# Optimization experiments

Measured on AMD Instinct MI355X. Metric: run time of the kernel, lower is better.

The kernel has to match this reference:

```python
import jax, jax.numpy as jnp
import numpy as np

N_NODES = 100000
N_EDGES = 1600000
F = 64          # node_features (in == out for EvolveGCNO)
HID = 64        # hidden_size


def setup_inputs() -> dict:
    key = jax.random.key(0)
    ks = jax.random.split(key, 12)
    s = 1.0 / np.sqrt(F)
    inp = {
        "x": jax.random.normal(ks[0], (N_NODES, F), dtype=jnp.float32),
        "edge_index": jax.random.randint(ks[1], (2, N_EDGES), 0, N_NODES, dtype=jnp.int64),
        "edge_weight": jax.random.uniform(ks[2], (N_EDGES,), dtype=jnp.float32),
        # evolving GCN weight (initial_weight of EvolveGCNO)
        "W0": jax.random.uniform(ks[3], (F, F), jnp.float32, -s, s),
        # GRU (input_size=F, hidden_size=F): gates ordered r, z, n
        "gru_Wi": jax.random.uniform(ks[4], (3 * F, F), jnp.float32, -s, s),
        "gru_Wh": jax.random.uniform(ks[5], (3 * F, F), jnp.float32, -s, s),
        "gru_bi": jax.random.uniform(ks[6], (3 * F,), jnp.float32, -s, s),
        "gru_bh": jax.random.uniform(ks[7], (3 * F,), jnp.float32, -s, s),
        # projection F -> HID and head HID -> 1
        "proj_W": jax.random.uniform(ks[8], (HID, F), jnp.float32, -s, s),
        "proj_b": jax.random.uniform(ks[9], (HID,), jnp.float32, -s, s),
        "lin_W": jax.random.uniform(ks[10], (1, HID), jnp.float32, -1.0 / np.sqrt(HID), 1.0 / np.sqrt(HID)),
        "lin_b": jax.random.uniform(ks[11], (1,), jnp.float32, -1.0 / np.sqrt(HID), 1.0 / np.sqrt(HID)),
    }
    return inp


def reference(x, edge_index, edge_weight, W0, gru_Wi, gru_Wh, gru_bi, gru_bh,
              proj_W, proj_b, lin_W, lin_b):
    N = x.shape[0]
    # --- EvolveGCNO weight evolution: one GRU step, rows of W0 are both input and hidden ---
    gi = W0 @ gru_Wi.T + gru_bi  # [F, 3F]
    gh = W0 @ gru_Wh.T + gru_bh  # [F, 3F]
    i_r, i_z, i_n = jnp.split(gi, 3, axis=1)
    h_r, h_z, h_n = jnp.split(gh, 3, axis=1)
    r = jax.nn.sigmoid(i_r + h_r)
    z = jax.nn.sigmoid(i_z + h_z)
    n = jnp.tanh(i_n + r * h_n)
    W = (1.0 - z) * n + z * W0  # evolved GCN weight [F, F]

    # --- GCNConv with fixed evolved W: X' = D^-1/2 (A + I) D^-1/2 (X W) ---
    xw = x @ W  # [N, F]
    src, dst = edge_index[0], edge_index[1]
    loop = jnp.arange(N)
    src2 = jnp.concatenate([src, loop])
    dst2 = jnp.concatenate([dst, loop])
    w2 = jnp.concatenate([edge_weight, jnp.ones((N,), xw.dtype)])  # self-loop weight 1
    deg = jax.ops.segment_sum(w2, dst2, num_segments=N)
    dinv = jnp.where(deg > 0, jax.lax.rsqrt(deg), 0.0)
    norm = dinv[src2] * w2 * dinv[dst2]  # [E + N]
    h = jax.ops.segment_sum(xw[src2] * norm[:, None], dst2, num_segments=N)  # [N, F]

    # --- MLP head (dropout is identity in eval) ---
    h = jax.nn.relu(h @ proj_W.T + proj_b)
    return h @ lin_W.T + lin_b  # [N, 1]
```

## Files before the change

### kernel.cpp

```cpp
#include <hip/hip_runtime.h>
#include <stdint.h>

#define FDIM 64
#define BINSH 6
#define NBINS 1563
#define BCAP 1536
#define OVCAP 8192
#define PSTAGE 4096

__device__ __forceinline__ float bf2f(unsigned int u) {
    union { float f; uint32_t i; } v; v.i = (u & 0xFFFFu) << 16; return v.f;
}
__device__ __forceinline__ unsigned short f2bf(float f) {
    union { float f; uint32_t i; } v; v.f = f;
    uint32_t u = v.i;
    u += 0x7FFFu + ((u >> 16) & 1u);
    return (unsigned short)(u >> 16);
}

__global__ __launch_bounds__(256) void k_sentinel(float* out, int N, float val) {
    int n = blockIdx.x * 256 + threadIdx.x;
    if (n < N) out[n] = (n == 0) ? val : 0.f;
}

__global__ __launch_bounds__(64) void k_evolve(
    const float* __restrict__ W0, const float* __restrict__ Wi,
    const float* __restrict__ Wh, const float* __restrict__ bi,
    const float* __restrict__ bh, float* __restrict__ W) {
    int i = blockIdx.x;
    int j = threadIdx.x;
    __shared__ float w0s[64];
    w0s[j] = W0[i * 64 + j];
    __syncthreads();
    float a0 = 0.f, a1 = 0.f, a2 = 0.f, b0 = 0.f, b1 = 0.f, b2 = 0.f;
#pragma unroll 8
    for (int k = 0; k < 64; k++) {
        float w0k = w0s[k];
        a0 += w0k * Wi[(j)       * 64 + k];
        a1 += w0k * Wi[(64 + j)  * 64 + k];
        a2 += w0k * Wi[(128 + j) * 64 + k];
        b0 += w0k * Wh[(j)       * 64 + k];
        b1 += w0k * Wh[(64 + j)  * 64 + k];
        b2 += w0k * Wh[(128 + j) * 64 + k];
    }
    float ir = a0 + bi[j],        hr = b0 + bh[j];
    float iz = a1 + bi[64 + j],   hz = b1 + bh[64 + j];
    float in_ = a2 + bi[128 + j], hn = b2 + bh[128 + j];
    float r = 1.f / (1.f + expf(-(ir + hr)));
    float z = 1.f / (1.f + expf(-(iz + hz)));
    float n = tanhf(in_ + r * hn);
    W[i * 64 + j] = (1.f - z) * n + z * w0s[j];
}

__global__ __launch_bounds__(64) void k_matM(
    const float* __restrict__ W, const float* __restrict__ projW,
    float* __restrict__ M) {
    int k = blockIdx.x;
    int j = threadIdx.x;
    __shared__ float wr[64];
    wr[j] = W[k * 64 + j];
    __syncthreads();
    float s = 0.f;
#pragma unroll 8
    for (int q = 0; q < 64; q++) s += wr[q] * projW[j * 64 + q];
    M[k * 64 + j] = s;
}

__global__ __launch_bounds__(256) void k_xm(
    const float* __restrict__ x, const float* __restrict__ M,
    unsigned short* __restrict__ xm, int N) {
    __shared__ float xs[64 * 68];
    __shared__ float ms[64 * 68];
    int t  = threadIdx.x;
    int nb = blockIdx.x * 64;
#pragma unroll
    for (int i = 0; i < 4; i++) {
        int lin = i * 1024 + t * 4;
        int row = lin >> 6, col = lin & 63;
        int node = nb + row;
        float4 v = make_float4(0.f, 0.f, 0.f, 0.f);
        if (node < N) v = *(const float4*)(x + (size_t)node * 64 + col);
        *(float4*)&xs[row * 68 + col] = v;
        *(float4*)&ms[row * 68 + col] = *(const float4*)(M + lin);
    }
    __syncthreads();
    int tj = t & 15, tn = t >> 4;
    float acc[4][4] = {};
    for (int k = 0; k < 64; k += 4) {
        float4 xv[4], mv[4];
#pragma unroll
        for (int nn = 0; nn < 4; nn++) xv[nn] = *(const float4*)&xs[(tn * 4 + nn) * 68 + k];
#pragma unroll
        for (int kk = 0; kk < 4; kk++) mv[kk] = *(const float4*)&ms[(k + kk) * 68 + tj * 4];
#pragma unroll
        for (int nn = 0; nn < 4; nn++) {
            const float* xp = (const float*)&xv[nn];
#pragma unroll
            for (int kk = 0; kk < 4; kk++) {
                float xk = xp[kk];
                const float* mp = (const float*)&mv[kk];
                acc[nn][0] += xk * mp[0];
                acc[nn][1] += xk * mp[1];
                acc[nn][2] += xk * mp[2];
                acc[nn][3] += xk * mp[3];
            }
        }
    }
#pragma unroll
    for (int nn = 0; nn < 4; nn++) {
        int node = nb + tn * 4 + nn;
        if (node < N) {
            ushort4 o;
            o.x = f2bf(acc[nn][0]); o.y = f2bf(acc[nn][1]);
            o.z = f2bf(acc[nn][2]); o.w = f2bf(acc[nn][3]);
            *(ushort4*)&xm[(size_t)node * 64 + tj * 4] = o;
        }
    }
}

__global__ __launch_bounds__(1024) void k_part(
    const int* __restrict__ src, const int* __restrict__ dst,
    const float* __restrict__ ew, int* __restrict__ gcnt,
    int2* __restrict__ part, int* __restrict__ ovf_cnt,
    int* __restrict__ ovs, int* __restrict__ ovd, float* __restrict__ ovw,
    int E) {
    __shared__ int  hist[NBINS];
    __shared__ int  scn[NBINS];
    __shared__ int  lcur[NBINS];
    __shared__ int2 stage[PSTAGE];
    __shared__ unsigned short sbin[PSTAGE];
    int t = threadIdx.x;
    for (int b = t; b < NBINS; b += 1024) hist[b] = 0;
    __syncthreads();
    int e0 = blockIdx.x * PSTAGE;
    int cnt = E - e0; if (cnt > PSTAGE) cnt = PSTAGE;
    for (int i = t; i < cnt; i += 1024) atomicAdd(&hist[dst[e0 + i] >> BINSH], 1);
    __syncthreads();
    for (int b = t; b < NBINS; b += 1024) scn[b] = hist[b];
    __syncthreads();
    for (int off = 1; off < NBINS; off <<= 1) {
        int i1 = t, i2 = t + 1024;
        int a1 = (i1 < NBINS && i1 >= off) ? scn[i1 - off] : 0;
        int a2 = (i2 < NBINS && i2 >= off) ? scn[i2 - off] : 0;
        __syncthreads();
        if (i1 < NBINS) scn[i1] += a1;
        if (i2 < NBINS) scn[i2] += a2;
        __syncthreads();
    }
    for (int b = t; b < NBINS; b += 1024) {
        int h = hist[b];
        int lbase = scn[b] - h;
        int gb = h ? atomicAdd(&gcnt[b], h) : 0;
        lcur[b] = lbase;
        hist[b] = gb - lbase;
    }
    __syncthreads();
    for (int i = t; i < cnt; i += 1024) {
        int e = e0 + i;
        int d = dst[e];
        int b = d >> BINSH;
        int p = atomicAdd(&lcur[b], 1);
        stage[p] = make_int2(src[e] | ((d & 63) << 20), __float_as_int(ew[e]));
        sbin[p] = (unsigned short)b;
    }
    __syncthreads();
    for (int i = t; i < cnt; i += 1024) {
        int b = sbin[i];
        int2 e = stage[i];
        int p = i + hist[b];
        if (p < BCAP) {
            part[(size_t)b * BCAP + p] = e;
        } else {
            int op = atomicAdd(ovf_cnt, 1);
            if (op < OVCAP) {
                ovs[op] = e.x & 0xFFFFF;
                ovd[op] = (b << BINSH) | ((e.x >> 20) & 63);
                ovw[op] = __int_as_float(e.y);
            }
        }
    }
}

__global__ __launch_bounds__(256) void k_deg2(
    const int* __restrict__ gcnt, const int2* __restrict__ part,
    const int* __restrict__ ovf_cnt, const int* __restrict__ ovd,
    const float* __restrict__ ovw,
    float* __restrict__ deg, float* __restrict__ dinv, int N) {
    __shared__ float dl[64];
    int t = threadIdx.x, b = blockIdx.x;
    if (t < 64) dl[t] = 1.0f;
    __syncthreads();
    int c = gcnt[b]; if (c > BCAP) c = BCAP;
    const int2* pe = part + (size_t)b * BCAP;
    for (int i = t; i < c; i += 256) {
        int2 e = pe[i];
        atomicAdd(&dl[(e.x >> 20) & 63], __int_as_float(e.y));
    }
    int m = *ovf_cnt; if (m > OVCAP) m = OVCAP;
    for (int i = t; i < m; i += 256) {
        int d = ovd[i];
        if ((d >> BINSH) == b) atomicAdd(&dl[d & 63], ovw[i]);
    }
    __syncthreads();
    int n = b * 64 + t;
    if (t < 64 && n < N) {
        float d = dl[t];
        deg[n] = d;
        dinv[n] = d > 0.f ? rsqrtf(d) : 0.f;
    }
}

__global__ __launch_bounds__(256) void k_gf(
    const unsigned short* __restrict__ xm, const float* __restrict__ dinv,
    const int* __restrict__ gcnt, const int2* __restrict__ part,
    const float* __restrict__ projB, const float* __restrict__ linW,
    const float* __restrict__ linB, const int* __restrict__ ovf_cnt,
    const int* __restrict__ ovs, const int* __restrict__ ovd,
    const float* __restrict__ ovw, float* __restrict__ out, int N) {
    __shared__ int  lcnt[64];
    __shared__ int  loff[65];
    __shared__ int  lcur[64];
    __shared__ int2 ledge[BCAP];
    __shared__ float pbs[64], lws[64];
    int t = threadIdx.x, b = blockIdx.x;
    if (t < 64) { lcnt[t] = 0; pbs[t] = projB[t]; lws[t] = linW[t]; }
    __syncthreads();
    int c = gcnt[b]; if (c > BCAP) c = BCAP;
    const int2* pe = part + (size_t)b * BCAP;
    for (int i = t; i < c; i += 256) {
        atomicAdd(&lcnt[(pe[i].x >> 20) & 63], 1);
    }
    __syncthreads();
    if (t == 0) {
        int o = 0;
#pragma unroll 16
        for (int k = 0; k < 64; k++) { loff[k] = o; o += lcnt[k]; }
        loff[64] = o;
    }
    __syncthreads();
    if (t < 64) lcur[t] = loff[t];
    __syncthreads();
    for (int i = t; i < c; i += 256) {
        int2 e = pe[i];
        int s = e.x & 0xFFFFF;
        float nw = dinv[s] * __int_as_float(e.y);
        int p = atomicAdd(&lcur[(e.x >> 20) & 63], 1);
        ledge[p] = make_int2(e.x, __float_as_int(nw));
    }
    __syncthreads();
    int m = *ovf_cnt; if (m > OVCAP) m = OVCAP;
    float lb = linB[0];
    int wv = t >> 6, lane = t & 63, eg = lane >> 4, fq = lane & 15, f = fq * 4;
    for (int nl = wv; nl < 64; nl += 4) {
        int n = b * 64 + nl;
        if (n >= N) continue;
        float dn = dinv[n];
        int beg = loff[nl], end = loff[nl + 1];
        float ax = 0.f, ay = 0.f, az = 0.f, aw = 0.f;
        float bx = 0.f, by = 0.f, bz = 0.f, bw = 0.f;
        int i = beg + eg;
        for (; i + 4 < end; i += 8) {
            int2 e0 = ledge[i];
            int2 e1 = ledge[i + 4];
            int s0 = e0.x & 0xFFFFF, s1 = e1.x & 0xFFFFF;
            uint2 u0 = *(const uint2*)&xm[(size_t)s0 * 64 + f];
            uint2 u1 = *(const uint2*)&xm[(size_t)s1 * 64 + f];
            float nm0 = __int_as_float(e0.y);
            float nm1 = __int_as_float(e1.y);
            ax += nm0 * bf2f(u0.x);       ay += nm0 * bf2f(u0.x >> 16);
            az += nm0 * bf2f(u0.y);       aw += nm0 * bf2f(u0.y >> 16);
            bx += nm1 * bf2f(u1.x);       by += nm1 * bf2f(u1.x >> 16);
            bz += nm1 * bf2f(u1.y);       bw += nm1 * bf2f(u1.y >> 16);
        }
        for (; i < end; i += 4) {
            int2 e = ledge[i];
            int s = e.x & 0xFFFFF;
            float nm = __int_as_float(e.y);
            uint2 u = *(const uint2*)&xm[(size_t)s * 64 + f];
            ax += nm * bf2f(u.x); ay += nm * bf2f(u.x >> 16);
            az += nm * bf2f(u.y); aw += nm * bf2f(u.y >> 16);
        }
        ax += bx; ay += by; az += bz; aw += bw;
        ax *= dn; ay *= dn; az *= dn; aw *= dn;
        ax += __shfl_xor(ax, 16); ay += __shfl_xor(ay, 16);
        az += __shfl_xor(az, 16); aw += __shfl_xor(aw, 16);
        ax += __shfl_xor(ax, 32); ay += __shfl_xor(ay, 32);
        az += __shfl_xor(az, 32); aw += __shfl_xor(aw, 32);
        if (eg == 0) {
            {
                uint2 u = *(const uint2*)&xm[(size_t)n * 64 + f];
                float sl = dn * dn;
                ax += sl * bf2f(u.x); ay += sl * bf2f(u.x >> 16);
                az += sl * bf2f(u.y); aw += sl * bf2f(u.y >> 16);
            }
            for (int q = 0; q < m; q++) {
                if (ovd[q] == n) {
                    int s = ovs[q];
                    float nm = dinv[s] * ovw[q] * dn;
                    uint2 u = *(const uint2*)&xm[(size_t)s * 64 + f];
                    ax += nm * bf2f(u.x); ay += nm * bf2f(u.x >> 16);
                    az += nm * bf2f(u.y); aw += nm * bf2f(u.y >> 16);
                }
            }
            float v0 = ax + pbs[f],     v1 = ay + pbs[f + 1];
            float v2 = az + pbs[f + 2], v3 = aw + pbs[f + 3];
            float s = (v0 > 0.f ? v0 : 0.f) * lws[f]
                    + (v1 > 0.f ? v1 : 0.f) * lws[f + 1]
                    + (v2 > 0.f ? v2 : 0.f) * lws[f + 2]
                    + (v3 > 0.f ? v3 : 0.f) * lws[f + 3];
            s += __shfl_xor(s, 1); s += __shfl_xor(s, 2);
            s += __shfl_xor(s, 4); s += __shfl_xor(s, 8);
            if (fq == 0) out[n] = s + lb;
        }
    }
}

extern "C" void kernel_launch(void* const* d_in, const int* in_sizes, int n_in,
                              void* d_out, int out_size, void* d_ws, size_t ws_size,
                              hipStream_t stream) {
    const float* x   = (const float*)d_in[0];
    const int*   ei  = (const int*)d_in[1];
    const float* ew  = (const float*)d_in[2];
    const float* W0  = (const float*)d_in[3];
    const float* gWi = (const float*)d_in[4];
    const float* gWh = (const float*)d_in[5];
    const float* gbi = (const float*)d_in[6];
    const float* gbh = (const float*)d_in[7];
    const float* pW  = (const float*)d_in[8];
    const float* pb  = (const float*)d_in[9];
    const float* lW  = (const float*)d_in[10];
    const float* lb  = (const float*)d_in[11];
    float* out = (float*)d_out;

    static const int EXPSZ[12] = {6400000, 3200000, 1600000, 4096, 12288, 12288,
                                  192, 192, 4096, 64, 64, 1};
    int mism = -1;
    for (int i = 0; i < 12 && i < n_in; i++)
        if (in_sizes[i] != EXPSZ[i]) { mism = i; break; }
    if (mism >= 0) {
        k_sentinel<<<(out_size + 255) / 256, 256, 0, stream>>>(out, out_size,
                                                               ldexpf(1.f, 30 + 3 * mism));
        return;
    }

    int N = in_sizes[0] / FDIM;
    int E = in_sizes[1] / 2;
    const int* src = ei;
    const int* dst = ei + E;

    char* wsb = (char*)d_ws;
    float* W       = (float*)(wsb);
    float* M       = (float*)(wsb + (16u << 10));
    int*   gcnt    = (int*)  (wsb + (32u << 10));
    int*   ovf_cnt = (int*)  (wsb + (39u << 10));
    int*   ovs     = (int*)  (wsb + (44u << 10));
    int*   ovd     = (int*)  (wsb + (76u << 10));
    float* ovw     = (float*)(wsb + (108u << 10));
    float* deg     = (float*)(wsb + (512u << 10));
    float* dinv    = (float*)(wsb + (1u << 20));
    int2*  part    = (int2*) (wsb + (2u << 20));
    unsigned short* xm = (unsigned short*)(wsb + (22u << 20));

    hipMemsetAsync(gcnt, 0, (8u << 10), stream);

    k_evolve<<<64, 64, 0, stream>>>(W0, gWi, gWh, gbi, gbh, W);
    k_matM<<<64, 64, 0, stream>>>(W, pW, M);
    k_xm<<<NBINS, 256, 0, stream>>>(x, M, xm, N);
    k_part<<<(E + PSTAGE - 1) / PSTAGE, 1024, 0, stream>>>(src, dst, ew, gcnt, part,
                                                           ovf_cnt, ovs, ovd, ovw, E);
    k_deg2<<<NBINS, 256, 0, stream>>>(gcnt, part, ovf_cnt, ovd, ovw, deg, dinv, N);
    k_gf<<<NBINS, 256, 0, stream>>>(xm, dinv, gcnt, part, pb, lW, lb,
                                    ovf_cnt, ovs, ovd, ovw, out, N);
}
```

Measured before the change: 206.6 us.

## Fuse GRU evolve with projection, drop memset, simplify edge partitioning

```diff
diff --git a/kernel.cpp b/kernel.cpp
--- a/kernel.cpp
+++ b/kernel.cpp
@@ -6,7 +6,7 @@
 #define NBINS 1563
 #define BCAP 1536
 #define OVCAP 8192
-#define PSTAGE 4096
+#define PSTAGE 8192
 
 __device__ __forceinline__ float bf2f(unsigned int u) {
     union { float f; uint32_t i; } v; v.i = (u & 0xFFFFu) << 16; return v.f;
@@ -23,13 +23,18 @@
     if (n < N) out[n] = (n == 0) ? val : 0.f;
 }
 
-__global__ __launch_bounds__(64) void k_evolve(
+__global__ __launch_bounds__(64) void k_evolveM(
     const float* __restrict__ W0, const float* __restrict__ Wi,
     const float* __restrict__ Wh, const float* __restrict__ bi,
-    const float* __restrict__ bh, float* __restrict__ W) {
+    const float* __restrict__ bh, const float* __restrict__ projW,
+    float* __restrict__ M, int* __restrict__ gcnt, int* __restrict__ ovf_cnt) {
     int i = blockIdx.x;
     int j = threadIdx.x;
+    int g = i * 64 + j;
+    if (g < NBINS) gcnt[g] = 0;
+    if (g == NBINS) *ovf_cnt = 0;
     __shared__ float w0s[64];
+    __shared__ float wrow[64];
     w0s[j] = W0[i * 64 + j];
     __syncthreads();
     float a0 = 0.f, a1 = 0.f, a2 = 0.f, b0 = 0.f, b1 = 0.f, b2 = 0.f;
@@ -49,21 +54,12 @@
     float r = 1.f / (1.f + expf(-(ir + hr)));
     float z = 1.f / (1.f + expf(-(iz + hz)));
     float n = tanhf(in_ + r * hn);
-    W[i * 64 + j] = (1.f - z) * n + z * w0s[j];
-}
-
-__global__ __launch_bounds__(64) void k_matM(
-    const float* __restrict__ W, const float* __restrict__ projW,
-    float* __restrict__ M) {
-    int k = blockIdx.x;
-    int j = threadIdx.x;
-    __shared__ float wr[64];
-    wr[j] = W[k * 64 + j];
+    wrow[j] = (1.f - z) * n + z * w0s[j];
     __syncthreads();
     float s = 0.f;
 #pragma unroll 8
-    for (int q = 0; q < 64; q++) s += wr[q] * projW[j * 64 + q];
-    M[k * 64 + j] = s;
+    for (int q = 0; q < 64; q++) s += wrow[q] * projW[j * 64 + q];
+    M[i * 64 + j] = s;
 }
 
 __global__ __launch_bounds__(256) void k_xm(
@@ -124,11 +120,8 @@
     int2* __restrict__ part, int* __restrict__ ovf_cnt,
     int* __restrict__ ovs, int* __restrict__ ovd, float* __restrict__ ovw,
     int E) {
-    __shared__ int  hist[NBINS];
-    __shared__ int  scn[NBINS];
-    __shared__ int  lcur[NBINS];
-    __shared__ int2 stage[PSTAGE];
-    __shared__ unsigned short sbin[PSTAGE];
+    __shared__ int hist[NBINS];
+    __shared__ int lcur[NBINS];
     int t = threadIdx.x;
     for (int b = t; b < NBINS; b += 1024) hist[b] = 0;
     __syncthreads();
@@ -136,23 +129,9 @@
     int cnt = E - e0; if (cnt > PSTAGE) cnt = PSTAGE;
     for (int i = t; i < cnt; i += 1024) atomicAdd(&hist[dst[e0 + i] >> BINSH], 1);
     __syncthreads();
-    for (int b = t; b < NBINS; b += 1024) scn[b] = hist[b];
-    __syncthreads();
-    for (int off = 1; off < NBINS; off <<= 1) {
-        int i1 = t, i2 = t + 1024;
-        int a1 = (i1 < NBINS && i1 >= off) ? scn[i1 - off] : 0;
-        int a2 = (i2 < NBINS && i2 >= off) ? scn[i2 - off] : 0;
-        __syncthreads();
-        if (i1 < NBINS) scn[i1] += a1;
-        if (i2 < NBINS) scn[i2] += a2;
-        __syncthreads();
-    }
     for (int b = t; b < NBINS; b += 1024) {
         int h = hist[b];
-        int lbase = scn[b] - h;
-        int gb = h ? atomicAdd(&gcnt[b], h) : 0;
-        lcur[b] = lbase;
-        hist[b] = gb - lbase;
+        lcur[b] = h ? atomicAdd(&gcnt[b], h) : 0;
     }
     __syncthreads();
     for (int i = t; i < cnt; i += 1024) {
@@ -160,22 +139,15 @@
         int d = dst[e];
         int b = d >> BINSH;
         int p = atomicAdd(&lcur[b], 1);
-        stage[p] = make_int2(src[e] | ((d & 63) << 20), __float_as_int(ew[e]));
-        sbin[p] = (unsigned short)b;
-    }
-    __syncthreads();
-    for (int i = t; i < cnt; i += 1024) {
-        int b = sbin[i];
-        int2 e = stage[i];
-        int p = i + hist[b];
         if (p < BCAP) {
-            part[(size_t)b * BCAP + p] = e;
+            part[(size_t)b * BCAP + p] = make_int2(src[e] | ((d & 63) << 20),
+                                                   __float_as_int(ew[e]));
         } else {
             int op = atomicAdd(ovf_cnt, 1);
             if (op < OVCAP) {
-                ovs[op] = e.x & 0xFFFFF;
-                ovd[op] = (b << BINSH) | ((e.x >> 20) & 63);
-                ovw[op] = __int_as_float(e.y);
+                ovs[op] = src[e];
+                ovd[op] = d;
+                ovw[op] = ew[e];
             }
         }
     }
@@ -349,8 +321,7 @@
     const int* dst = ei + E;
 
     char* wsb = (char*)d_ws;
-    float* W       = (float*)(wsb);
-    float* M       = (float*)(wsb + (16u << 10));
+    float* M       = (float*)(wsb);
     int*   gcnt    = (int*)  (wsb + (32u << 10));
     int*   ovf_cnt = (int*)  (wsb + (39u << 10));
     int*   ovs     = (int*)  (wsb + (44u << 10));
@@ -361,10 +332,7 @@
     int2*  part    = (int2*) (wsb + (2u << 20));
     unsigned short* xm = (unsigned short*)(wsb + (22u << 20));
 
-    hipMemsetAsync(gcnt, 0, (8u << 10), stream);
-
-    k_evolve<<<64, 64, 0, stream>>>(W0, gWi, gWh, gbi, gbh, W);
-    k_matM<<<64, 64, 0, stream>>>(W, pW, M);
+    k_evolveM<<<64, 64, 0, stream>>>(W0, gWi, gWh, gbi, gbh, pW, M, gcnt, ovf_cnt);
     k_xm<<<NBINS, 256, 0, stream>>>(x, M, xm, N);
     k_part<<<(E + PSTAGE - 1) / PSTAGE, 1024, 0, stream>>>(src, dst, ew, gcnt, part,
                                                            ovf_cnt, ovs, ovd, ovw, E);
```

Result: faster. 195.9 us (-5.2%).
